# Performance work log

Measured on AMD Instinct MI355X. Metric: run time of the kernel, lower is better.

Reference implementation:

```python
import jax, jax.numpy as jnp
import numpy as np

B, S, D, H, DH, F = 2, 2048, 1024, 16, 64, 4096
K = 2048  # number of selected tokens (capacity_gamma=0.5 of B*S)
EPS = 1e-6
ROPE_THETA = 10000.0


def setup_inputs() -> dict:
    key = jax.random.key(0)
    ks = jax.random.split(key, 12)
    w = lambda k, shp: jax.random.normal(k, shp, dtype=jnp.float32) * 0.02
    # K unique flat indices into the B*S token grid (every other token -> unique, sorted)
    sel_flat = jnp.arange(K, dtype=jnp.int64) * 2
    return {
        "hidden_states": jax.random.normal(ks[0], (B, S, D), dtype=jnp.float32),
        "gating_signal": jax.random.uniform(ks[1], (B, S), dtype=jnp.float32),
        "sel_flat": sel_flat,
        "position_ids": jnp.tile(jnp.arange(S, dtype=jnp.int64), (B, 1)),
        "ln1_w": jnp.ones((D,), jnp.float32),
        "ln2_w": jnp.ones((D,), jnp.float32),
        "wq": w(ks[2], (D, H * DH)), "bq": jnp.zeros((H * DH,), jnp.float32),
        "wk": w(ks[3], (D, H * DH)), "bk": jnp.zeros((H * DH,), jnp.float32),
        "wv": w(ks[4], (D, H * DH)), "bv": jnp.zeros((H * DH,), jnp.float32),
        "wo": w(ks[5], (H * DH, D)),
        "w_gate": w(ks[6], (D, F)),
        "w_up": w(ks[7], (D, F)),
        "w_down": w(ks[8], (F, D)),
    }


def _rmsnorm(x, w):
    var = jnp.mean(jnp.square(x), axis=-1, keepdims=True)
    return x * jax.lax.rsqrt(var + EPS) * w


def _rope(x, pos):
    # x: [K, H, DH], pos: [K]
    half = DH // 2
    inv_freq = 1.0 / (ROPE_THETA ** (jnp.arange(half, dtype=jnp.float32) / half))
    ang = pos.astype(jnp.float32)[:, None] * inv_freq  # [K, half]
    cos = jnp.cos(ang)[:, None, :]
    sin = jnp.sin(ang)[:, None, :]
    x1, x2 = x[..., :half], x[..., half:]
    return jnp.concatenate([x1 * cos - x2 * sin, x2 * cos + x1 * sin], axis=-1)


def reference(hidden_states, gating_signal, sel_flat, position_ids,
              ln1_w, ln2_w, wq, bq, wk, bk, wv, bv, wo, w_gate, w_up, w_down):
    b_idx = sel_flat // S
    t_idx = sel_flat % S

    # --- gather selected tokens ---
    x = hidden_states[b_idx, t_idx]          # [K, D]
    g = gating_signal[b_idx, t_idx]          # [K]
    pos = position_ids[b_idx, t_idx]         # [K]

    # --- Qwen2 block on the selected tokens (single sequence of length K) ---
    h = _rmsnorm(x, ln1_w)
    q = _rope((h @ wq + bq).reshape(K, H, DH), pos)
    k = _rope((h @ wk + bk).reshape(K, H, DH), pos)
    v = (h @ wv + bv).reshape(K, H, DH)

    scores = jnp.einsum("qhd,khd->hqk", q, k) / np.sqrt(DH)  # [H, K, K]
    causal = jnp.tril(jnp.ones((K, K), dtype=bool))
    scores = jnp.where(causal, scores, jnp.finfo(scores.dtype).min)
    probs = jax.nn.softmax(scores, axis=-1)
    attn = jnp.einsum("hqk,khd->qhd", probs, v).reshape(K, H * DH) @ wo

    x1 = x + attn
    h2 = _rmsnorm(x1, ln2_w)
    mlp = (jax.nn.silu(h2 @ w_gate) * (h2 @ w_up)) @ w_down
    y = x1 + mlp                              # processed tokens [K, D]

    # --- gated residual scatter-back ---
    updated = x + (y - x) * g[:, None]
    return hidden_states.at[b_idx, t_idx].set(updated)
```

## Files before the change

### kernel.cpp

```cpp
#include <hip/hip_runtime.h>
#include <hip/hip_bf16.h>
#include <stdint.h>

#define K_TOK 2048
#define D_DIM 1024
#define H_N   16
#define DH_N  64
#define F_DIM 4096
#define S_SEQ 2048

typedef __attribute__((ext_vector_type(4))) float f32x4;
typedef __attribute__((ext_vector_type(8))) short bf16x8;

__device__ __forceinline__ float bf2f(ushort u) {
  union { unsigned u; float f; } c; c.u = ((unsigned)u) << 16; return c.f;
}
__device__ __forceinline__ ushort f2bf(float f) {
  union { float f; unsigned u; } c; c.f = f;
  unsigned x = c.u + 0x7fffu + ((c.u >> 16) & 1u);
  return (ushort)(x >> 16);
}

#define GLOAD_LDS16(GP, LP)                                                   \
  __builtin_amdgcn_global_load_lds(                                           \
      (const __attribute__((address_space(1))) unsigned int*)(GP),            \
      (__attribute__((address_space(3))) unsigned int*)(LP), 16, 0, 0)

__global__ void copy_out_k(const float4* __restrict__ src, float4* __restrict__ dst, int n4) {
  int idx = blockIdx.x * blockDim.x + threadIdx.x;
  int stride = gridDim.x * blockDim.x;
  for (; idx < n4; idx += stride) dst[idx] = src[idx];
}

__global__ void prep_bias(const float* __restrict__ bq, const float* __restrict__ bk,
                          const float* __restrict__ bv, float* __restrict__ dst) {
  int i = blockIdx.x * 256 + threadIdx.x;
  if (i < 3072) dst[i] = (i < 1024) ? bq[i] : (i < 2048 ? bk[i - 1024] : bv[i - 2048]);
}

__global__ __launch_bounds__(256) void transpose_conv64(const float* __restrict__ src,
                                                        ushort* __restrict__ dst,
                                                        int R, int C, int mul, int add, int ldd) {
  __shared__ float tile[64][65];
  int nbx = C >> 6;
  int bx = blockIdx.x % nbx, by = blockIdx.x / nbx;
  int c0 = bx << 6, r0 = by << 6;
  int tx = threadIdx.x & 15, ty = threadIdx.x >> 4;
#pragma unroll
  for (int i = 0; i < 4; ++i) {
    float4 v = *(const float4*)&src[(size_t)(r0 + ty + i * 16) * C + c0 + tx * 4];
    *(float4*)&tile[ty + i * 16][tx * 4] = v;
  }
  __syncthreads();
#pragma unroll
  for (int i = 0; i < 4; ++i) {
    int c = ty + i * 16;
    ushort4 o;
    o.x = f2bf(tile[tx * 4 + 0][c]);
    o.y = f2bf(tile[tx * 4 + 1][c]);
    o.z = f2bf(tile[tx * 4 + 2][c]);
    o.w = f2bf(tile[tx * 4 + 3][c]);
    *(ushort4*)&dst[(size_t)((c0 + c) * mul + add) * ldd + r0 + tx * 4] = o;
  }
}

__global__ __launch_bounds__(256) void gather_ln1(
    const float* __restrict__ hs, const float* __restrict__ gating,
    const int* __restrict__ sel32, const int* __restrict__ pos32,
    const float* __restrict__ w,
    float* __restrict__ xbuf, ushort* __restrict__ hbuf,
    float* __restrict__ gbuf, int* __restrict__ rowb, int* __restrict__ rowt,
    int* __restrict__ rowpos) {
  int i = blockIdx.x, tid = threadIdx.x;
  __shared__ float red[4];
  bool is64 = (sel32[1] == 0 && sel32[3] == 0 && sel32[5] == 0);
  int sel = is64 ? sel32[2 * i] : sel32[i];
  int b = sel >> 11;
  int t = sel & 2047;
  const float4* src = (const float4*)(hs + ((size_t)b * S_SEQ + t) * D_DIM);
  float4 v = src[tid];
  float ss = v.x * v.x + v.y * v.y + v.z * v.z + v.w * v.w;
  for (int off = 32; off; off >>= 1) ss += __shfl_xor(ss, off);
  if ((tid & 63) == 0) red[tid >> 6] = ss;
  __syncthreads();
  float tot = red[0] + red[1] + red[2] + red[3];
  float rms = rsqrtf(tot * (1.f / 1024.f) + 1e-6f);
  ((float4*)(xbuf + (size_t)i * D_DIM))[tid] = v;
  float4 lw = ((const float4*)w)[tid];
  ushort4 hv;
  hv.x = f2bf(v.x * rms * lw.x); hv.y = f2bf(v.y * rms * lw.y);
  hv.z = f2bf(v.z * rms * lw.z); hv.w = f2bf(v.w * rms * lw.w);
  *(ushort4*)&hbuf[(size_t)i * D_DIM + tid * 4] = hv;
  if (tid == 0) {
    rowb[i] = b; rowt[i] = t;
    bool is64p = (pos32[1] == 0 && pos32[3] == 0 && pos32[5] == 0);
    int pidx = b * S_SEQ + t;
    rowpos[i] = is64p ? pos32[2 * pidx] : pos32[pidx];
    gbuf[i] = gating[pidx];
  }
}

__global__ __launch_bounds__(256) void rmsnorm_ep1(const float* __restrict__ xbuf,
                                                   const float* __restrict__ pb,
                                                   const float* __restrict__ w,
                                                   float* __restrict__ x1out,
                                                   ushort* __restrict__ h2out) {
  int i = blockIdx.x, tid = threadIdx.x;
  __shared__ float red[4];
  size_t e = (size_t)i * D_DIM;
  float4 v = ((const float4*)(xbuf + e))[tid];
  float4 p0 = ((const float4*)(pb + e))[tid];
  float4 p1 = ((const float4*)(pb + 2097152 + e))[tid];
  v.x += p0.x + p1.x; v.y += p0.y + p1.y; v.z += p0.z + p1.z; v.w += p0.w + p1.w;
  ((float4*)(x1out + e))[tid] = v;
  float ss = v.x * v.x + v.y * v.y + v.z * v.z + v.w * v.w;
  for (int off = 32; off; off >>= 1) ss += __shfl_xor(ss, off);
  if ((tid & 63) == 0) red[tid >> 6] = ss;
  __syncthreads();
  float tot = red[0] + red[1] + red[2] + red[3];
  float rms = rsqrtf(tot * (1.f / 1024.f) + 1e-6f);
  float4 lw = ((const float4*)w)[tid];
  ushort4 hv;
  hv.x = f2bf(v.x * rms * lw.x); hv.y = f2bf(v.y * rms * lw.y);
  hv.z = f2bf(v.z * rms * lw.z); hv.w = f2bf(v.w * rms * lw.w);
  *(ushort4*)&h2out[e + tid * 4] = hv;
}

__global__ __launch_bounds__(256) void ep3_k(const float* __restrict__ pb,
                                             const float* __restrict__ x1b,
                                             const float* __restrict__ xbuf,
                                             const float* __restrict__ gbuf,
                                             const int* __restrict__ rowb,
                                             const int* __restrict__ rowt,
                                             float* __restrict__ out) {
  int idx = blockIdx.x * 256 + threadIdx.x;
  int row = idx >> 8, c4 = idx & 255;
  size_t e = (size_t)row * D_DIM + c4 * 4;
  float4 s0 = *(const float4*)(pb + e);
  float4 s1 = *(const float4*)(pb + 2097152 + e);
  float4 s2 = *(const float4*)(pb + 2 * 2097152 + e);
  float4 s3 = *(const float4*)(pb + 3 * 2097152 + e);
  float4 x = *(const float4*)(xbuf + e);
  float4 x1 = *(const float4*)(x1b + e);
  float g = gbuf[row];
  float4 r;
  r.x = x.x + (x1.x + s0.x + s1.x + s2.x + s3.x - x.x) * g;
  r.y = x.y + (x1.y + s0.y + s1.y + s2.y + s3.y - x.y) * g;
  r.z = x.z + (x1.z + s0.z + s1.z + s2.z + s3.z - x.z) * g;
  r.w = x.w + (x1.w + s0.w + s1.w + s2.w + s3.w - x.w) * g;
  *(float4*)(out + ((size_t)rowb[row] * S_SEQ + rowt[row]) * D_DIM + c4 * 4) = r;
}

template <int MODE>
__global__ __launch_bounds__(256) void gemm_bt(
    const ushort* __restrict__ A, const ushort* __restrict__ BT,
    int M, int N, int ldk, int kdeff, int per,
    const float* __restrict__ bias,
    ushort* __restrict__ outb, float* __restrict__ outf) {
  __shared__ ushort lA[128 * 64];
  __shared__ ushort lB[128 * 64];
  int tid = threadIdx.x;
  int lane = tid & 63, wid = tid >> 6;
  int kidx = blockIdx.x / per;
  int bid = blockIdx.x % per;
  int nbn = N >> 7;
  int tm = bid / nbn, tn = bid % nbn;
  int wr = wid >> 1, wc = wid & 1;
  f32x4 acc[4][4];
#pragma unroll
  for (int m = 0; m < 4; ++m)
#pragma unroll
    for (int n = 0; n < 4; ++n) acc[m][n] = (f32x4){0.f, 0.f, 0.f, 0.f};

  const ushort* Ab = A + (size_t)(tm * 128) * ldk + (size_t)kidx * kdeff;
  const ushort* Bb = BT + (size_t)(tn * 128) * ldk + (size_t)kidx * kdeff;
  int lr = lane & 15, lg = lane >> 4;
  int prow = lane >> 3;
  int pch = lane & 7;

  for (int k0 = 0; k0 < kdeff; k0 += 64) {
    __syncthreads();
#pragma unroll
    for (int p = 0; p < 4; ++p) {
      int row = p * 32 + wid * 8 + prow;
      int g = pch ^ (row & 7);
      GLOAD_LDS16(Ab + (size_t)row * ldk + k0 + g * 8, &lA[(p * 32 + wid * 8) * 64]);
      GLOAD_LDS16(Bb + (size_t)row * ldk + k0 + g * 8, &lB[(p * 32 + wid * 8) * 64]);
    }
    __syncthreads();
#pragma unroll
    for (int ks = 0; ks < 2; ++ks) {
      bf16x8 af[4], bfv[4];
#pragma unroll
      for (int m = 0; m < 4; ++m) {
        int row = wr * 64 + m * 16 + lr;
        af[m] = *(const bf16x8*)((const char*)lA + row * 128 +
                                 ((ks * 64 + lg * 16) ^ ((row & 7) << 4)));
      }
#pragma unroll
      for (int n = 0; n < 4; ++n) {
        int row = wc * 64 + n * 16 + lr;
        bfv[n] = *(const bf16x8*)((const char*)lB + row * 128 +
                                  ((ks * 64 + lg * 16) ^ ((row & 7) << 4)));
      }
#pragma unroll
      for (int m = 0; m < 4; ++m)
#pragma unroll
        for (int n = 0; n < 4; ++n)
          acc[m][n] = __builtin_amdgcn_mfma_f32_16x16x32_bf16(af[m], bfv[n], acc[m][n], 0, 0, 0);
    }
  }

#pragma unroll
  for (int m = 0; m < 4; ++m) {
#pragma unroll
    for (int n = 0; n < 4; ++n) {
#pragma unroll
      for (int r = 0; r < 4; ++r) {
        int gr = tm * 128 + wr * 64 + m * 16 + lg * 4 + r;
        int gc = tn * 128 + wc * 64 + n * 16 + lr;
        float val = acc[m][n][r];
        if (MODE == 0) {
          outb[(size_t)gr * N + gc] = f2bf(val + bias[gc]);
        } else {
          outf[((size_t)kidx * M + gr) * N + gc] = val;
        }
      }
    }
  }
}

__global__ __launch_bounds__(512, 2) void gemm256_gu(const ushort* __restrict__ A,
                                                     const ushort* __restrict__ BT,
                                                     ushort* __restrict__ outb) {
  __shared__ ushort lA[2][256 * 32];
  __shared__ ushort lB[2][256 * 32];
  int tid = threadIdx.x, lane = tid & 63, wid = tid >> 6;
  int bid = blockIdx.x;
  int sb = (bid & 7) * 32 + (bid >> 3);
  int tm = sb >> 5, tn = sb & 31;
  int wm = wid >> 2, wn = wid & 3;
  int lr = lane & 15, lg = lane >> 4;
  const ushort* Ab = A + (size_t)(tm * 256) * 1024;
  const ushort* Bb = BT + (size_t)(tn * 256) * 1024;
  int srow = lane >> 2, sch = lane & 3;

  f32x4 acc[8][4];
#pragma unroll
  for (int m = 0; m < 8; ++m)
#pragma unroll
    for (int n = 0; n < 4; ++n) acc[m][n] = (f32x4){0.f, 0.f, 0.f, 0.f};

#define STAGE_GU(bi, t)                                                        \
  {                                                                            \
    int k0 = (t) * 32;                                                         \
    _Pragma("unroll") for (int j = 0; j < 2; ++j) {                            \
      int R = j * 128 + wid * 16;                                              \
      int row = R + srow;                                                      \
      int g = sch ^ (row & 3);                                                 \
      GLOAD_LDS16(Ab + (size_t)row * 1024 + k0 + g * 8, &lA[bi][R * 32]);      \
      GLOAD_LDS16(Bb + (size_t)row * 1024 + k0 + g * 8, &lB[bi][R * 32]);      \
    }                                                                          \
  }

  STAGE_GU(0, 0);
  STAGE_GU(1, 1);
  asm volatile("s_waitcnt vmcnt(4)" ::: "memory");
  __syncthreads();

  for (int t = 0; t < 32; ++t) {
    int c = t & 1;
    bf16x8 af[8], bfr[4];
#pragma unroll
    for (int m = 0; m < 8; ++m) {
      int row = wm * 128 + m * 16 + lr;
      af[m] = *(const bf16x8*)((const char*)&lA[c][0] + row * 64 +
                               ((lg * 16) ^ ((row & 3) << 4)));
    }
#pragma unroll
    for (int n = 0; n < 4; ++n) {
      int row = wn * 64 + n * 16 + lr;
      bfr[n] = *(const bf16x8*)((const char*)&lB[c][0] + row * 64 +
                                ((lg * 16) ^ ((row & 3) << 4)));
    }
    asm volatile("s_waitcnt lgkmcnt(0)" ::: "memory");
    __syncthreads();
    if (t + 2 < 32) STAGE_GU(c, t + 2);
    __builtin_amdgcn_sched_barrier(0);
    __builtin_amdgcn_s_setprio(1);
#pragma unroll
    for (int m = 0; m < 8; ++m)
#pragma unroll
      for (int n = 0; n < 4; ++n)
        acc[m][n] = __builtin_amdgcn_mfma_f32_16x16x32_bf16(af[m], bfr[n], acc[m][n], 0, 0, 0);
    __builtin_amdgcn_s_setprio(0);
    if (t + 1 < 32) {
      if (t + 2 < 32)
        asm volatile("s_waitcnt vmcnt(4)" ::: "memory");
      else
        asm volatile("s_waitcnt vmcnt(0)" ::: "memory");
      __syncthreads();
    }
  }

#pragma unroll
  for (int m = 0; m < 8; ++m) {
#pragma unroll
    for (int n = 0; n < 4; ++n) {
#pragma unroll
      for (int r = 0; r < 4; ++r) {
        int gr = tm * 256 + wm * 128 + m * 16 + lg * 4 + r;
        int gc = tn * 256 + wn * 64 + n * 16 + lr;
        float val = acc[m][n][r];
        float other = __shfl_xor(val, 1);
        if (!(lane & 1)) {
          float g = val, u = other;
          float a = g / (1.f + __expf(-g)) * u;
          outb[(size_t)gr * (F_DIM) + (gc >> 1)] = f2bf(a);
        }
      }
    }
  }
#undef STAGE_GU
}

__global__ __launch_bounds__(256) void rope_kernel(const ushort* __restrict__ qkv,
                                                   const int* __restrict__ rowpos,
                                                   ushort* __restrict__ qr,
                                                   ushort* __restrict__ kr) {
  int idx = blockIdx.x * 256 + threadIdx.x;
  int i = idx >> 9;
  int rem = idx & 511;
  int h = rem >> 5, d = rem & 31;
  float pos = (float)rowpos[i];
  float inv = __expf(-(float)d * (9.210340371976184f / 32.0f));
  float ang = pos * inv;
  float sn, cs;
  __sincosf(ang, &sn, &cs);
  size_t base = (size_t)i * 3072;
  float q1 = bf2f(qkv[base + h * 64 + d]);
  float q2 = bf2f(qkv[base + h * 64 + 32 + d]);
  float k1 = bf2f(qkv[base + 1024 + h * 64 + d]);
  float k2 = bf2f(qkv[base + 1024 + h * 64 + 32 + d]);
  size_t ob = ((size_t)h * K_TOK + i) * DH_N;
  qr[ob + d] = f2bf((q1 * cs - q2 * sn) * 0.125f);
  qr[ob + 32 + d] = f2bf((q2 * cs + q1 * sn) * 0.125f);
  kr[ob + d] = f2bf(k1 * cs - k2 * sn);
  kr[ob + 32 + d] = f2bf(k2 * cs + k1 * sn);
}

__global__ __launch_bounds__(256) void vtrans_k(const ushort* __restrict__ qkv,
                                                ushort* __restrict__ vt) {
  __shared__ ushort tile[32][33];
  int bx = blockIdx.x & 63, by = blockIdx.x >> 6;
  int i0 = bx << 5, c0 = by << 5;
  int tx = threadIdx.x & 31, ty = threadIdx.x >> 5;
#pragma unroll
  for (int j = 0; j < 32; j += 8)
    tile[ty + j][tx] = qkv[(size_t)(i0 + ty + j) * 3072 + 2048 + c0 + tx];
  __syncthreads();
#pragma unroll
  for (int j = 0; j < 32; j += 8)
    vt[(size_t)(c0 + ty + j) * K_TOK + i0 + tx] = tile[tx][ty + j];
}

__global__ __launch_bounds__(256) void attn_mfma(const ushort* __restrict__ qr,
                                                 const ushort* __restrict__ kr,
                                                 const ushort* __restrict__ vt,
                                                 ushort* __restrict__ ows,
                                                 float* __restrict__ mlws) {
  __shared__ ushort ktile[2][64 * 64];
  __shared__ ushort vtile[2][64 * 64];
  __shared__ ushort pbuf[4][16 * 64];
  int tid = threadIdx.x, lane = tid & 63, wid = tid >> 6;
  int bid = blockIdx.x;
  int h = bid / 144;
  int rem = 143 - (bid % 144);
  int g = 0;
  while (rem >= 2 * (g + 1) * (g + 2)) ++g;
  int rem2 = rem - 2 * g * (g + 1);
  int qt = (g << 2) + rem2 / (g + 1);
  int ci = rem2 % (g + 1);
  int slot = h * 144 + rem;
  int q0 = qt << 6;
  int t0 = ci << 2;
  int t1 = min(t0 + 3, qt);

  const ushort* Kh = kr + (size_t)h * K_TOK * DH_N;
  const ushort* Vh = vt + (size_t)h * DH_N * K_TOK;
  int lr = lane & 15, lg = lane >> 4;
  int qbase = q0 + wid * 16;

  bf16x8 qf[2];
  const ushort* Qp = qr + ((size_t)h * K_TOK + qbase + lr) * DH_N + lg * 8;
  qf[0] = *(const bf16x8*)(Qp);
  qf[1] = *(const bf16x8*)(Qp + 32);

  f32x4 oa[4];
  float mreg[4], lreg[4];
#pragma unroll
  for (int ct = 0; ct < 4; ++ct) oa[ct] = (f32x4){0.f, 0.f, 0.f, 0.f};
#pragma unroll
  for (int r = 0; r < 4; ++r) { mreg[r] = -1e30f; lreg[r] = 0.f; }

  char* pws = (char*)&pbuf[wid][0];
  int srow8 = lane >> 3, schunk = lane & 7;

  auto stage = [&](int bi, int kb) {
#pragma unroll
    for (int j = 0; j < 2; ++j) {
      int rbase = wid * 16 + j * 8;
      int row = rbase + srow8;
      int gch = schunk ^ (row & 7);
      GLOAD_LDS16(Kh + (size_t)(kb + row) * DH_N + gch * 8, &ktile[bi][rbase * 64]);
      GLOAD_LDS16(Vh + (size_t)row * K_TOK + kb + gch * 8, &vtile[bi][rbase * 64]);
    }
  };

  stage(0, t0 << 6);
  int cur = 0;
  for (int t = t0; t <= t1; ++t) {
    int kb = t << 6;
    __syncthreads();
    if (t < t1) stage(cur ^ 1, (t + 1) << 6);

    const char* kt = (const char*)&ktile[cur][0];
    const char* vtl = (const char*)&vtile[cur][0];

    f32x4 sa[4];
#pragma unroll
    for (int ct = 0; ct < 4; ++ct) sa[ct] = (f32x4){0.f, 0.f, 0.f, 0.f};
#pragma unroll
    for (int s = 0; s < 2; ++s) {
#pragma unroll
      for (int ct = 0; ct < 4; ++ct) {
        int row = ct * 16 + lr;
        bf16x8 kf = *(const bf16x8*)(kt + row * 128 + ((s * 64 + lg * 16) ^ ((row & 7) << 4)));
        sa[ct] = __builtin_amdgcn_mfma_f32_16x16x32_bf16(qf[s], kf, sa[ct], 0, 0, 0);
      }
    }

#pragma unroll
    for (int r = 0; r < 4; ++r) {
      int q = qbase + lg * 4 + r;
      int prow = lg * 4 + r;
      float sv[4];
      float mx = mreg[r];
#pragma unroll
      for (int ct = 0; ct < 4; ++ct) {
        int key = kb + ct * 16 + lr;
        float x = sa[ct][r];
        sv[ct] = (key <= q) ? x : -1e30f;
        mx = fmaxf(mx, sv[ct]);
      }
      mx = fmaxf(mx, __shfl_xor(mx, 1));
      mx = fmaxf(mx, __shfl_xor(mx, 2));
      mx = fmaxf(mx, __shfl_xor(mx, 4));
      mx = fmaxf(mx, __shfl_xor(mx, 8));
      float resc = __expf(mreg[r] - mx);
      float ps = 0.f;
#pragma unroll
      for (int ct = 0; ct < 4; ++ct) {
        float p = __expf(sv[ct] - mx);
        ps += p;
        *(ushort*)(pws + prow * 128 + ((ct * 32 + lr * 2) ^ ((prow & 7) << 4))) = f2bf(p);
      }
      ps += __shfl_xor(ps, 1);
      ps += __shfl_xor(ps, 2);
      ps += __shfl_xor(ps, 4);
      ps += __shfl_xor(ps, 8);
      lreg[r] = lreg[r] * resc + ps;
      mreg[r] = mx;
#pragma unroll
      for (int ct = 0; ct < 4; ++ct) oa[ct][r] *= resc;
    }

    bf16x8 pf[2];
#pragma unroll
    for (int s = 0; s < 2; ++s)
      pf[s] = *(const bf16x8*)(pws + lr * 128 + ((s * 64 + lg * 16) ^ ((lr & 7) << 4)));
#pragma unroll
    for (int s = 0; s < 2; ++s) {
#pragma unroll
      for (int ct = 0; ct < 4; ++ct) {
        int row = ct * 16 + lr;
        bf16x8 vf = *(const bf16x8*)(vtl + row * 128 + ((s * 64 + lg * 16) ^ ((row & 7) << 4)));
        oa[ct] = __builtin_amdgcn_mfma_f32_16x16x32_bf16(pf[s], vf, oa[ct], 0, 0, 0);
      }
    }
    cur ^= 1;
  }

#pragma unroll
  for (int ct = 0; ct < 4; ++ct) {
#pragma unroll
    for (int r = 0; r < 4; ++r) {
      int prow = wid * 16 + lg * 4 + r;
      ows[(size_t)slot * 4096 + prow * 64 + ct * 16 + lr] = f2bf(oa[ct][r]);
    }
  }
  if (lr == 0) {
#pragma unroll
    for (int r = 0; r < 4; ++r) {
      int prow = wid * 16 + lg * 4 + r;
      mlws[(size_t)slot * 128 + prow] = mreg[r];
      mlws[(size_t)slot * 128 + 64 + prow] = lreg[r];
    }
  }
}

__global__ __launch_bounds__(256) void attn_combine(const ushort* __restrict__ ows,
                                                    const float* __restrict__ mlws,
                                                    ushort* __restrict__ aout) {
  int bid = blockIdx.x;
  int h = bid & 15, qt = bid >> 4;
  int g = qt >> 2;
  int nc = g + 1;
  int base = h * 144 + 2 * g * (g + 1) + (qt & 3) * nc;
  int tid = threadIdx.x;
  int row = tid >> 2, c0 = (tid & 3) * 16;
  float M = -1e30f;
  for (int i = 0; i < nc; ++i)
    M = fmaxf(M, mlws[(size_t)(base + i) * 128 + row]);
  float L = 0.f;
  float acc[16];
#pragma unroll
  for (int j = 0; j < 16; ++j) acc[j] = 0.f;
  for (int i = 0; i < nc; ++i) {
    size_t sl = (size_t)(base + i);
    float w = __expf(mlws[sl * 128 + row] - M);
    L += mlws[sl * 128 + 64 + row] * w;
    const bf16x8* op = (const bf16x8*)(ows + sl * 4096 + row * 64 + c0);
    bf16x8 v0 = op[0], v1 = op[1];
#pragma unroll
    for (int j = 0; j < 8; ++j) acc[j] += bf2f(((ushort)v0[j])) * w;
#pragma unroll
    for (int j = 0; j < 8; ++j) acc[8 + j] += bf2f(((ushort)v1[j])) * w;
  }
  float inv = 1.f / L;
  int q = qt * 64 + row;
  ushort* dst = aout + (size_t)q * D_DIM + h * DH_N + c0;
#pragma unroll
  for (int j = 0; j < 16; ++j) dst[j] = f2bf(acc[j] * inv);
}

extern "C" void kernel_launch(void* const* d_in, const int* in_sizes, int n_in,
                              void* d_out, int out_size, void* d_ws, size_t ws_size,
                              hipStream_t stream) {
  const float* hs = (const float*)d_in[0];
  const float* gating = (const float*)d_in[1];
  const int* sel32 = (const int*)d_in[2];
  const int* pos32 = (const int*)d_in[3];
  const float* ln1w = (const float*)d_in[4];
  const float* ln2w = (const float*)d_in[5];
  const float* wq = (const float*)d_in[6];
  const float* bq = (const float*)d_in[7];
  const float* wk = (const float*)d_in[8];
  const float* bk = (const float*)d_in[9];
  const float* wv = (const float*)d_in[10];
  const float* bv = (const float*)d_in[11];
  const float* wo = (const float*)d_in[12];
  const float* wg = (const float*)d_in[13];
  const float* wu = (const float*)d_in[14];
  const float* wd = (const float*)d_in[15];
  float* out = (float*)d_out;

  char* wsb = (char*)d_ws;
  size_t off = 0;
  auto alloc = [&](size_t bytes) -> void* {
    void* p = wsb + off;
    off += (bytes + 255) & ~(size_t)255;
    return p;
  };
  ushort* qkvT = (ushort*)alloc(3072ull * 1024 * 2);
  ushort* woT = (ushort*)alloc(1024ull * 1024 * 2);
  ushort* guT = (ushort*)alloc(8192ull * 1024 * 2);
  ushort* wdT = (ushort*)alloc(1024ull * 4096 * 2);
  float* biasqkv = (float*)alloc(3072 * 4);
  float* xbuf = (float*)alloc(2048ull * 1024 * 4);
  ushort* hbuf = (ushort*)alloc(2048ull * 1024 * 2);
  ushort* qkv = (ushort*)alloc(2048ull * 3072 * 2);
  ushort* qrb = (ushort*)alloc(16ull * 2048 * 64 * 2);
  ushort* krb = (ushort*)alloc(16ull * 2048 * 64 * 2);
  ushort* vtb = (ushort*)alloc(16ull * 64 * 2048 * 2);
  ushort* aoutb = (ushort*)alloc(2048ull * 1024 * 2);
  float* pbuf = (float*)hbuf;
  float* x1b = (float*)alloc(2048ull * 1024 * 4);
  ushort* h2b = (ushort*)alloc(2048ull * 1024 * 2);
  ushort* actb = (ushort*)alloc(2048ull * 4096 * 2);
  ushort* aows = (ushort*)x1b;
  float* amlws = (float*)((char*)x1b + 2304ull * 4096 * 2);
  float* gbuf = (float*)alloc(2048 * 4);
  int* rowb = (int*)alloc(2048 * 4);
  int* rowt = (int*)alloc(2048 * 4);
  int* rowpos = (int*)alloc(2048 * 4);
  if (off > ws_size) return;

  copy_out_k<<<2048, 256, 0, stream>>>((const float4*)hs, (float4*)out, (2 * S_SEQ * D_DIM) / 4);
  prep_bias<<<12, 256, 0, stream>>>(bq, bk, bv, biasqkv);
  transpose_conv64<<<256, 256, 0, stream>>>(wq, qkvT, 1024, 1024, 1, 0, 1024);
  transpose_conv64<<<256, 256, 0, stream>>>(wk, qkvT + 1024 * 1024, 1024, 1024, 1, 0, 1024);
  transpose_conv64<<<256, 256, 0, stream>>>(wv, qkvT + 2048 * 1024, 1024, 1024, 1, 0, 1024);
  transpose_conv64<<<256, 256, 0, stream>>>(wo, woT, 1024, 1024, 1, 0, 1024);
  transpose_conv64<<<1024, 256, 0, stream>>>(wg, guT, 1024, 4096, 2, 0, 1024);
  transpose_conv64<<<1024, 256, 0, stream>>>(wu, guT, 1024, 4096, 2, 1, 1024);
  transpose_conv64<<<1024, 256, 0, stream>>>(wd, wdT, 4096, 1024, 1, 0, 4096);
  gather_ln1<<<2048, 256, 0, stream>>>(hs, gating, sel32, pos32, ln1w, xbuf, hbuf, gbuf, rowb,
                                       rowt, rowpos);
  gemm_bt<0><<<16 * 24, 256, 0, stream>>>(hbuf, qkvT, 2048, 3072, 1024, 1024, 16 * 24, biasqkv,
                                          qkv, nullptr);
  rope_kernel<<<4096, 256, 0, stream>>>(qkv, rowpos, qrb, krb);
  vtrans_k<<<2048, 256, 0, stream>>>(qkv, vtb);
  attn_mfma<<<16 * 144, 256, 0, stream>>>(qrb, krb, vtb, aows, amlws);
  attn_combine<<<512, 256, 0, stream>>>(aows, amlws, aoutb);
  gemm_bt<4><<<2 * 16 * 8, 256, 0, stream>>>(aoutb, woT, 2048, 1024, 1024, 512, 16 * 8, nullptr,
                                             nullptr, pbuf);
  rmsnorm_ep1<<<2048, 256, 0, stream>>>(xbuf, pbuf, ln2w, x1b, h2b);
  gemm256_gu<<<256, 512, 0, stream>>>(h2b, guT, actb);
  gemm_bt<4><<<4 * 16 * 8, 256, 0, stream>>>(actb, wdT, 2048, 1024, 4096, 1024, 16 * 8, nullptr,
                                             nullptr, pbuf);
  ep3_k<<<2048, 256, 0, stream>>>(pbuf, x1b, xbuf, gbuf, rowb, rowt, out);
}
```

Measured before the change: 229.9 us.

## Deepen gate/up GEMM K-tile to 64 and split A fragment loads around MFMAs

The fused gate/up GEMM now stages 64-wide K slices (16 iterations instead of 32), using an 8-way XOR swizzle for LDS. Each iteration loads the B fragments and half of the A fragments, runs MFMAs on that half, then loads the second half of A while the first MFMAs run. This halves the number of barriers and lets LDS reads overlap with compute. The block-to-tile mapping also changes from a swizzled order to a simple one. The cost is doubled LDS use (128KB per block at launch bounds 512,2), which may limit occupancy.

```diff
diff --git a/kernel.cpp b/kernel.cpp
--- a/kernel.cpp
+++ b/kernel.cpp
@@ -233,17 +233,15 @@
 __global__ __launch_bounds__(512, 2) void gemm256_gu(const ushort* __restrict__ A,
                                                      const ushort* __restrict__ BT,
                                                      ushort* __restrict__ outb) {
-  __shared__ ushort lA[2][256 * 32];
-  __shared__ ushort lB[2][256 * 32];
+  __shared__ ushort lA[2][256 * 64];
+  __shared__ ushort lB[2][256 * 64];
   int tid = threadIdx.x, lane = tid & 63, wid = tid >> 6;
   int bid = blockIdx.x;
-  int sb = (bid & 7) * 32 + (bid >> 3);
-  int tm = sb >> 5, tn = sb & 31;
+  int tm = bid & 7, tn = bid >> 3;
   int wm = wid >> 2, wn = wid & 3;
   int lr = lane & 15, lg = lane >> 4;
   const ushort* Ab = A + (size_t)(tm * 256) * 1024;
   const ushort* Bb = BT + (size_t)(tn * 256) * 1024;
-  int srow = lane >> 2, sch = lane & 3;
 
   f32x4 acc[8][4];
 #pragma unroll
@@ -251,55 +249,80 @@
 #pragma unroll
     for (int n = 0; n < 4; ++n) acc[m][n] = (f32x4){0.f, 0.f, 0.f, 0.f};
 
-#define STAGE_GU(bi, t)                                                        \
-  {                                                                            \
-    int k0 = (t) * 32;                                                         \
-    _Pragma("unroll") for (int j = 0; j < 2; ++j) {                            \
-      int R = j * 128 + wid * 16;                                              \
-      int row = R + srow;                                                      \
-      int g = sch ^ (row & 3);                                                 \
-      GLOAD_LDS16(Ab + (size_t)row * 1024 + k0 + g * 8, &lA[bi][R * 32]);      \
-      GLOAD_LDS16(Bb + (size_t)row * 1024 + k0 + g * 8, &lB[bi][R * 32]);      \
-    }                                                                          \
-  }
-
-  STAGE_GU(0, 0);
-  STAGE_GU(1, 1);
-  asm volatile("s_waitcnt vmcnt(4)" ::: "memory");
-  __syncthreads();
-
-  for (int t = 0; t < 32; ++t) {
+  int grow = lane >> 3;
+  int gsw = (lane & 7) ^ grow;
+
+  auto STG = [&](int bi, int t) {
+#pragma unroll
+    for (int r = 0; r < 4; ++r) {
+      int rb = wid * 4 + r;
+      int row = rb * 8 + grow;
+      GLOAD_LDS16(Ab + (size_t)row * 1024 + t * 64 + gsw * 8, &lA[bi][rb * 512]);
+      GLOAD_LDS16(Bb + (size_t)row * 1024 + t * 64 + gsw * 8, &lB[bi][rb * 512]);
+    }
+  };
+
+  STG(0, 0);
+  STG(1, 1);
+  asm volatile("s_waitcnt vmcnt(8)" ::: "memory");
+  __builtin_amdgcn_s_barrier();
+
+  for (int t = 0; t < 16; ++t) {
     int c = t & 1;
-    bf16x8 af[8], bfr[4];
-#pragma unroll
-    for (int m = 0; m < 8; ++m) {
-      int row = wm * 128 + m * 16 + lr;
-      af[m] = *(const bf16x8*)((const char*)&lA[c][0] + row * 64 +
-                               ((lg * 16) ^ ((row & 3) << 4)));
-    }
+    const char* bA = (const char*)&lA[c][0];
+    const char* bB = (const char*)&lB[c][0];
+    bf16x8 bfr[4][2], afh[4][2];
 #pragma unroll
     for (int n = 0; n < 4; ++n) {
       int row = wn * 64 + n * 16 + lr;
-      bfr[n] = *(const bf16x8*)((const char*)&lB[c][0] + row * 64 +
-                                ((lg * 16) ^ ((row & 3) << 4)));
+#pragma unroll
+      for (int kk = 0; kk < 2; ++kk)
+        bfr[n][kk] = *(const bf16x8*)(bB + row * 128 + ((kk * 64 + lg * 16) ^ ((lr & 7) << 4)));
+    }
+#pragma unroll
+    for (int m = 0; m < 4; ++m) {
+      int row = wm * 128 + m * 16 + lr;
+#pragma unroll
+      for (int kk = 0; kk < 2; ++kk)
+        afh[m][kk] = *(const bf16x8*)(bA + row * 128 + ((kk * 64 + lg * 16) ^ ((lr & 7) << 4)));
+    }
+    __builtin_amdgcn_s_setprio(1);
+#pragma unroll
+    for (int m = 0; m < 4; ++m)
+#pragma unroll
+      for (int n = 0; n < 4; ++n)
+#pragma unroll
+        for (int kk = 0; kk < 2; ++kk)
+          acc[m][n] = __builtin_amdgcn_mfma_f32_16x16x32_bf16(afh[m][kk], bfr[n][kk],
+                                                              acc[m][n], 0, 0, 0);
+    __builtin_amdgcn_s_setprio(0);
+#pragma unroll
+    for (int m = 0; m < 4; ++m) {
+      int row = wm * 128 + 64 + m * 16 + lr;
+#pragma unroll
+      for (int kk = 0; kk < 2; ++kk)
+        afh[m][kk] = *(const bf16x8*)(bA + row * 128 + ((kk * 64 + lg * 16) ^ ((lr & 7) << 4)));
     }
     asm volatile("s_waitcnt lgkmcnt(0)" ::: "memory");
-    __syncthreads();
-    if (t + 2 < 32) STAGE_GU(c, t + 2);
+    __builtin_amdgcn_s_barrier();
+    if (t + 2 < 16) STG(c, t + 2);
     __builtin_amdgcn_sched_barrier(0);
     __builtin_amdgcn_s_setprio(1);
 #pragma unroll
-    for (int m = 0; m < 8; ++m)
+    for (int m = 0; m < 4; ++m)
 #pragma unroll
       for (int n = 0; n < 4; ++n)
-        acc[m][n] = __builtin_amdgcn_mfma_f32_16x16x32_bf16(af[m], bfr[n], acc[m][n], 0, 0, 0);
+#pragma unroll
+        for (int kk = 0; kk < 2; ++kk)
+          acc[4 + m][n] = __builtin_amdgcn_mfma_f32_16x16x32_bf16(afh[m][kk], bfr[n][kk],
+                                                                  acc[4 + m][n], 0, 0, 0);
     __builtin_amdgcn_s_setprio(0);
-    if (t + 1 < 32) {
-      if (t + 2 < 32)
-        asm volatile("s_waitcnt vmcnt(4)" ::: "memory");
+    if (t < 15) {
+      if (t + 2 < 16)
+        asm volatile("s_waitcnt vmcnt(8)" ::: "memory");
       else
         asm volatile("s_waitcnt vmcnt(0)" ::: "memory");
-      __syncthreads();
+      __builtin_amdgcn_s_barrier();
     }
   }
 
@@ -321,7 +344,6 @@
       }
     }
   }
-#undef STAGE_GU
 }
 
 __global__ __launch_bounds__(256) void rope_kernel(const ushort* __restrict__ qkv,
```

Result: faster. 218.6 us (-4.9%).
